# Optimization experiments

Measured on AMD Instinct MI355X. Metric: run time of the kernel, lower is better.

Reference implementation:

```python
import jax, jax.numpy as jnp
import numpy as np

N_HEAD, D_K, D_V, EPS = 8, 64, 64, 1e-6


def setup_inputs() -> dict:
    key = jax.random.key(0)
    ks = jax.random.split(key, 7)
    b, n, t, d = 8, 4, 512, 512
    q = jax.random.normal(ks[0], (b, n, t, d), dtype=jnp.float32)
    k = jax.random.normal(ks[1], (b, n, t, d), dtype=jnp.float32)
    v = jax.random.normal(ks[2], (b, n, t, d), dtype=jnp.float32)
    s = 1.0 / np.sqrt(d)
    w_q = jax.random.normal(ks[3], (N_HEAD * D_K, d), dtype=jnp.float32) * s
    w_k = jax.random.normal(ks[4], (N_HEAD * D_K, d), dtype=jnp.float32) * s
    w_v = jax.random.normal(ks[5], (N_HEAD * D_V, d), dtype=jnp.float32) * s
    w_fc = jax.random.normal(ks[6], (d, N_HEAD * D_V), dtype=jnp.float32) * s
    ln_gamma = jnp.ones((d,), dtype=jnp.float32)
    ln_beta = jnp.zeros((d,), dtype=jnp.float32)
    return {"q": q, "k": k, "v": v, "w_q": w_q, "w_k": w_k, "w_v": w_v,
            "w_fc": w_fc, "ln_gamma": ln_gamma, "ln_beta": ln_beta}


def reference(q, k, v, w_q, w_k, w_v, w_fc, ln_gamma, ln_beta):
    b, n, t, d = q.shape
    B = b * n
    qf = q.reshape(B, t, d)
    kf = k.reshape(B, t, d)
    vf = v.reshape(B, t, d)
    residual = qf
    # projections -> [B, H, T, dk/dv]
    Q = jnp.einsum('btd,ed->bte', qf, w_q).reshape(B, t, N_HEAD, D_K).transpose(0, 2, 1, 3)
    K = jnp.einsum('btd,ed->bte', kf, w_k).reshape(B, t, N_HEAD, D_K).transpose(0, 2, 1, 3)
    V = jnp.einsum('btd,ed->bte', vf, w_v).reshape(B, t, N_HEAD, D_V).transpose(0, 2, 1, 3)
    # scaled dot-product attention (scale by sqrt(d_k) of q's last dim)
    scale = 1.0 / jnp.sqrt(jnp.asarray(D_K, dtype=Q.dtype))
    attn = jax.nn.softmax(jnp.einsum('bhqd,bhkd->bhqk', Q * scale, K), axis=-1)
    O = jnp.einsum('bhqk,bhkd->bhqd', attn, V)  # [B, H, T, dv]
    # merge heads, then the original's extra transpose+view (layout scramble)
    x = O.transpose(0, 2, 1, 3).reshape(B, t, N_HEAD * D_V)
    x = jnp.transpose(x, (0, 2, 1)).reshape(B, t, N_HEAD * D_V)
    x = jnp.einsum('bte,de->btd', x, w_fc)
    x = x + residual
    # LayerNorm(eps=1e-6)
    mu = jnp.mean(x, axis=-1, keepdims=True)
    var = jnp.var(x, axis=-1, keepdims=True)
    x = (x - mu) * jax.lax.rsqrt(var + EPS) * ln_gamma + ln_beta
    return x.reshape(b, n, t, d)
```

## Files before the change

kernel.cpp:

```cpp
#include <hip/hip_runtime.h>
#include <hip/hip_bf16.h>
#include <stdint.h>

typedef __attribute__((ext_vector_type(8))) short bf16x8;
typedef __attribute__((ext_vector_type(4))) float f32x4;
typedef unsigned int u32;

#define MFMA16(a,b,c) __builtin_amdgcn_mfma_f32_16x16x32_bf16((a),(b),(c),0,0,0)

__device__ __forceinline__ unsigned short f2bf(float f) {
    unsigned u = __float_as_uint(f);
    u = (u + 0x7FFFu + ((u >> 16) & 1u)) >> 16;
    return (unsigned short)u;
}
__device__ __forceinline__ float bf2f(unsigned short h) {
    return __uint_as_float(((unsigned)h) << 16);
}
__device__ __forceinline__ void gload16(const unsigned short* gp, unsigned short* lp) {
    __builtin_amdgcn_global_load_lds(
        (const __attribute__((address_space(1))) u32*)gp,
        (__attribute__((address_space(3))) u32*)lp, 16, 0, 0);
}
__device__ __forceinline__ int xcd_swz(int bid, int q8) {
    return (bid & 7) * q8 + (bid >> 3);
}


__global__ __launch_bounds__(256) void prep_w(
    const float* __restrict__ wq, const float* __restrict__ wk, const float* __restrict__ wv,
    const float* __restrict__ wfc, unsigned short* __restrict__ Wcat)
{
    const int c = blockIdx.x * 256 + threadIdx.x;
    const int w = c >> 15;
    const long off = (long)(c & 32767) * 8;
    const float* src = (w == 0) ? wq : (w == 1) ? wk : (w == 2) ? wv : wfc;
    unsigned short* dst = Wcat + (long)w * 262144;
    const float4 a = *(const float4*)(src + off);
    const float4 b = *(const float4*)(src + off + 4);
    uint4 pk;
    pk.x = (u32)f2bf(a.x) | ((u32)f2bf(a.y) << 16);
    pk.y = (u32)f2bf(a.z) | ((u32)f2bf(a.w) << 16);
    pk.z = (u32)f2bf(b.x) | ((u32)f2bf(b.y) << 16);
    pk.w = (u32)f2bf(b.z) | ((u32)f2bf(b.w) << 16);
    *(uint4*)(dst + off) = pk;
}

__global__ __launch_bounds__(256) void proj_kernel(
    const float* __restrict__ qf, const float* __restrict__ kf, const float* __restrict__ vf,
    const unsigned short* __restrict__ Wcat,
    unsigned short* __restrict__ Qb, unsigned short* __restrict__ Kb,
    unsigned short* __restrict__ Vt)
{
    __shared__ __align__(16) unsigned short As[2][128 * 64];
    __shared__ __align__(16) unsigned short Bs[2][128 * 64];

    const int work = xcd_swz(blockIdx.x, 192);
    const int x = work & 3, y = (work >> 2) & 127, z = work >> 9;
    const float* Af = (z == 0) ? qf : (z == 1) ? kf : vf;
    const unsigned short* Bm = Wcat + (size_t)z * 262144;
    unsigned short* out = (z == 0) ? Qb : (z == 1) ? Kb : Vt;
    const int mode = (z == 2) ? 1 : 0;
    const float scale = (z == 0) ? 0.125f : 1.0f;
    const int m0 = y * 128, n0 = x * 128;

    const int tid = threadIdx.x, wid = tid >> 6, lane = tid & 63;
    const int wm = wid >> 1, wn = wid & 1;
    const int g = lane >> 4, cc = lane & 15;

    f32x4 acc[4][4];
    #pragma unroll
    for (int a = 0; a < 4; a++)
        #pragma unroll
        for (int b = 0; b < 4; b++)
            acc[a][b] = (f32x4){0.f, 0.f, 0.f, 0.f};

    int sslot[4], srow[4], scd[4];
    #pragma unroll
    for (int j = 0; j < 4; j++) {
        const int s = j * 256 + wid * 64 + lane;
        sslot[j] = s; srow[j] = s >> 3; scd[j] = (s & 7) ^ ((s >> 3) & 7);
    }

    float4 ra[8];
    auto LOADA = [&](int k0) {
        #pragma unroll
        for (int j = 0; j < 4; j++) {
            const float* src = Af + (size_t)(m0 + srow[j]) * 512 + k0 + scd[j] * 8;
            ra[2 * j]     = *(const float4*)src;
            ra[2 * j + 1] = *(const float4*)(src + 4);
        }
    };
    auto WRITEA = [&](unsigned short* Asb) {
        #pragma unroll
        for (int j = 0; j < 4; j++) {
            uint4 pk;
            pk.x = (u32)f2bf(ra[2 * j].x)     | ((u32)f2bf(ra[2 * j].y) << 16);
            pk.y = (u32)f2bf(ra[2 * j].z)     | ((u32)f2bf(ra[2 * j].w) << 16);
            pk.z = (u32)f2bf(ra[2 * j + 1].x) | ((u32)f2bf(ra[2 * j + 1].y) << 16);
            pk.w = (u32)f2bf(ra[2 * j + 1].z) | ((u32)f2bf(ra[2 * j + 1].w) << 16);
            *(uint4*)(Asb + (size_t)sslot[j] * 8) = pk;
        }
    };
    auto STAGEB = [&](unsigned short* Bsb, int k0) {
        #pragma unroll
        for (int j = 0; j < 4; j++) {
            const int sb = j * 256 + wid * 64;
            gload16(Bm + (size_t)(n0 + srow[j]) * 512 + k0 + scd[j] * 8,
                    Bsb + (size_t)sb * 8);
        }
    };

    LOADA(0); STAGEB(Bs[0], 0); WRITEA(As[0]);
    __syncthreads();

    #pragma unroll
    for (int t = 0; t < 8; t++) {
        unsigned short* Ac = As[t & 1];
        unsigned short* Bc = Bs[t & 1];
        if (t < 7) {
            LOADA((t + 1) * 64);
            STAGEB(Bs[(t + 1) & 1], (t + 1) * 64);
        }

        #pragma unroll
        for (int kc = 0; kc < 2; kc++) {
            bf16x8 af[4], bfr[4];
            #pragma unroll
            for (int mf = 0; mf < 4; mf++) {
                const int r = wm * 64 + mf * 16 + cc;
                af[mf] = *(const bf16x8*)(Ac + r * 64 + (((kc * 4 + g) ^ (r & 7)) * 8));
            }
            #pragma unroll
            for (int nf = 0; nf < 4; nf++) {
                const int r = wn * 64 + nf * 16 + cc;
                bfr[nf] = *(const bf16x8*)(Bc + r * 64 + (((kc * 4 + g) ^ (r & 7)) * 8));
            }
            __builtin_amdgcn_s_setprio(1);
            #pragma unroll
            for (int mf = 0; mf < 4; mf++)
                #pragma unroll
                for (int nf = 0; nf < 4; nf++)
                    acc[mf][nf] = MFMA16(af[mf], bfr[nf], acc[mf][nf]);
            __builtin_amdgcn_s_setprio(0);
        }
        if (t < 7) WRITEA(As[(t + 1) & 1]);
        __syncthreads();
    }

    #pragma unroll
    for (int mf = 0; mf < 4; mf++) {
        const int rg = m0 + wm * 64 + mf * 16 + g * 4;
        const int t0 = rg & 511, bI = rg >> 9;
        #pragma unroll
        for (int nf = 0; nf < 4; nf++) {
            const int col = n0 + wn * 64 + nf * 16 + cc;
            const int h = col >> 6, dd = col & 63;
            if (mode == 0) {
                const size_t base = ((size_t)((bI * 8 + h) * 512 + t0)) * 64 + dd;
                #pragma unroll
                for (int i = 0; i < 4; i++)
                    out[base + (size_t)i * 64] = f2bf(acc[mf][nf][i] * scale);
            } else {
                const size_t base = ((size_t)((bI * 8 + h) * 64 + dd)) * 512 + t0;
                uint2 pk;
                pk.x = (u32)f2bf(acc[mf][nf][0]) | ((u32)f2bf(acc[mf][nf][1]) << 16);
                pk.y = (u32)f2bf(acc[mf][nf][2]) | ((u32)f2bf(acc[mf][nf][3]) << 16);
                *(uint2*)(out + base) = pk;
            }
        }
    }
}

__global__ __launch_bounds__(256) void fc_kernel(
    const unsigned short* __restrict__ Os, const unsigned short* __restrict__ Wfc,
    unsigned short* __restrict__ Y)
{
    __shared__ __align__(16) unsigned short As[2][128 * 64];
    __shared__ __align__(16) unsigned short Bs[2][128 * 64];
    const int work = xcd_swz(blockIdx.x, 64);
    const int n0 = (work & 3) * 128, m0 = (work >> 2) * 128;

    const int tid = threadIdx.x, wid = tid >> 6, lane = tid & 63;
    const int wm = wid >> 1, wn = wid & 1;
    const int g = lane >> 4, cc = lane & 15;

    f32x4 acc[4][4];
    #pragma unroll
    for (int a = 0; a < 4; a++)
        #pragma unroll
        for (int b = 0; b < 4; b++)
            acc[a][b] = (f32x4){0.f, 0.f, 0.f, 0.f};

    auto STAGE = [&](unsigned short* Asb, unsigned short* Bsb, int k0) {
        #pragma unroll
        for (int j = 0; j < 4; j++) {
            const int sb = j * 256 + wid * 64;
            const int s = sb + lane;
            const int r = s >> 3;
            const int cd = (s & 7) ^ (r & 7);
            gload16(Os  + (size_t)(m0 + r) * 512 + k0 + cd * 8, Asb + (size_t)sb * 8);
            gload16(Wfc + (size_t)(n0 + r) * 512 + k0 + cd * 8, Bsb + (size_t)sb * 8);
        }
    };

    STAGE(As[0], Bs[0], 0);
    __syncthreads();

    #pragma unroll
    for (int t = 0; t < 8; t++) {
        unsigned short* Ac = As[t & 1];
        unsigned short* Bc = Bs[t & 1];
        if (t < 7) STAGE(As[(t + 1) & 1], Bs[(t + 1) & 1], (t + 1) * 64);

        #pragma unroll
        for (int kc = 0; kc < 2; kc++) {
            bf16x8 af[4], bfr[4];
            #pragma unroll
            for (int mf = 0; mf < 4; mf++) {
                const int r = wm * 64 + mf * 16 + cc;
                af[mf] = *(const bf16x8*)(Ac + r * 64 + (((kc * 4 + g) ^ (r & 7)) * 8));
            }
            #pragma unroll
            for (int nf = 0; nf < 4; nf++) {
                const int r = wn * 64 + nf * 16 + cc;
                bfr[nf] = *(const bf16x8*)(Bc + r * 64 + (((kc * 4 + g) ^ (r & 7)) * 8));
            }
            __builtin_amdgcn_s_setprio(1);
            #pragma unroll
            for (int mf = 0; mf < 4; mf++)
                #pragma unroll
                for (int nf = 0; nf < 4; nf++)
                    acc[mf][nf] = MFMA16(af[mf], bfr[nf], acc[mf][nf]);
            __builtin_amdgcn_s_setprio(0);
        }
        __syncthreads();
    }

    #pragma unroll
    for (int mf = 0; mf < 4; mf++) {
        const int rg = m0 + wm * 64 + mf * 16 + g * 4;
        #pragma unroll
        for (int nf = 0; nf < 4; nf++) {
            const int col = n0 + wn * 64 + nf * 16 + cc;
            #pragma unroll
            for (int i = 0; i < 4; i++)
                Y[(size_t)(rg + i) * 512 + col] = f2bf(acc[mf][nf][i]);
        }
    }
}

__global__ __launch_bounds__(256) void attn_kernel(
    const unsigned short* __restrict__ Qb, const unsigned short* __restrict__ Kb,
    const unsigned short* __restrict__ Vt, unsigned short* __restrict__ Os)
{
    __shared__ __align__(16) unsigned short Ks[64 * 64];
    __shared__ __align__(16) unsigned short Vs[64 * 64];
    __shared__ __align__(16) unsigned short Ps[4 * 32 * 64];

    const int work = xcd_swz(blockIdx.x, 128);
    const int qt = work & 3, bh = work >> 2;
    const int tid = threadIdx.x;
    const int wid = tid >> 6, lane = tid & 63;
    const int g = lane >> 4, cc = lane & 15;

    const unsigned short* Qp = Qb + (size_t)bh * 512 * 64;
    const unsigned short* Kp = Kb + (size_t)bh * 512 * 64;
    const unsigned short* Vp = Vt + (size_t)bh * 64 * 512;

    const int q0 = qt * 128 + wid * 32;

    bf16x8 qf[2][2];
    #pragma unroll
    for (int mf = 0; mf < 2; mf++)
        #pragma unroll
        for (int kb = 0; kb < 2; kb++)
            qf[mf][kb] = *(const bf16x8*)(Qp + (size_t)(q0 + mf * 16 + cc) * 64 + kb * 32 + g * 8);

    f32x4 o[2][4];
    #pragma unroll
    for (int a = 0; a < 2; a++)
        #pragma unroll
        for (int b = 0; b < 4; b++)
            o[a][b] = (f32x4){0.f, 0.f, 0.f, 0.f};
    float lrun[2][4];
    #pragma unroll
    for (int a = 0; a < 2; a++)
        #pragma unroll
        for (int i = 0; i < 4; i++) lrun[a][i] = 0.f;

    const int sb = wid * 64;
    const int s1 = sb + lane, r1 = s1 >> 3, cd1 = (s1 & 7) ^ (r1 & 7);
    const int s2 = sb + 256 + lane, r2 = s2 >> 3, cd2 = (s2 & 7) ^ (r2 & 7);

    for (int kt = 0; kt < 8; kt++) {
        gload16(Kp + (size_t)(kt * 64 + r1) * 64 + cd1 * 8, Ks + (size_t)sb * 8);
        gload16(Kp + (size_t)(kt * 64 + r2) * 64 + cd2 * 8, Ks + (size_t)(sb + 256) * 8);
        gload16(Vp + (size_t)r1 * 512 + kt * 64 + cd1 * 8, Vs + (size_t)sb * 8);
        gload16(Vp + (size_t)r2 * 512 + kt * 64 + cd2 * 8, Vs + (size_t)(sb + 256) * 8);
        __syncthreads();

        f32x4 s[2][4];
        #pragma unroll
        for (int a = 0; a < 2; a++)
            #pragma unroll
            for (int b = 0; b < 4; b++)
                s[a][b] = (f32x4){0.f, 0.f, 0.f, 0.f};
        __builtin_amdgcn_s_setprio(1);
        #pragma unroll
        for (int nf = 0; nf < 4; nf++) {
            const int r = nf * 16 + cc;
            #pragma unroll
            for (int kb = 0; kb < 2; kb++) {
                bf16x8 kf = *(const bf16x8*)(Ks + r * 64 + (((kb * 4 + g) ^ (r & 7)) * 8));
                s[0][nf] = MFMA16(qf[0][kb], kf, s[0][nf]);
                s[1][nf] = MFMA16(qf[1][kb], kf, s[1][nf]);
            }
        }
        __builtin_amdgcn_s_setprio(0);

        unsigned short* Pw = Ps + wid * 32 * 64;
        #pragma unroll
        for (int mf = 0; mf < 2; mf++)
            #pragma unroll
            for (int i = 0; i < 4; i++) {
                float lacc = 0.f;
                #pragma unroll
                for (int nf = 0; nf < 4; nf++) {
                    float p = __expf(s[mf][nf][i]);
                    s[mf][nf][i] = p;
                    lacc += p;
                }
                lrun[mf][i] += lacc;
            }

        #pragma unroll
        for (int mf = 0; mf < 2; mf++)
            #pragma unroll
            for (int nf = 0; nf < 4; nf++) {
                const int c = nf * 16 + cc, csl = c >> 3, cin = c & 7;
                #pragma unroll
                for (int i = 0; i < 4; i++) {
                    const int row = mf * 16 + g * 4 + i;
                    Pw[row * 64 + ((csl ^ (row & 7)) * 8) + cin] = f2bf(s[mf][nf][i]);
                }
            }

        __builtin_amdgcn_s_setprio(1);
        #pragma unroll
        for (int kc = 0; kc < 2; kc++) {
            bf16x8 pa[2], vb[4];
            #pragma unroll
            for (int mf = 0; mf < 2; mf++) {
                const int r = mf * 16 + cc;
                pa[mf] = *(const bf16x8*)(Pw + r * 64 + (((kc * 4 + g) ^ (r & 7)) * 8));
            }
            #pragma unroll
            for (int vf = 0; vf < 4; vf++) {
                const int r = vf * 16 + cc;
                vb[vf] = *(const bf16x8*)(Vs + r * 64 + (((kc * 4 + g) ^ (r & 7)) * 8));
            }
            #pragma unroll
            for (int mf = 0; mf < 2; mf++)
                #pragma unroll
                for (int vf = 0; vf < 4; vf++)
                    o[mf][vf] = MFMA16(pa[mf], vb[vf], o[mf][vf]);
        }
        __builtin_amdgcn_s_setprio(0);
        __syncthreads();
    }

    const int b = bh >> 3, h = bh & 7;
    #pragma unroll
    for (int mf = 0; mf < 2; mf++) {
        int tq0 = q0 + mf * 16 + g * 4;
        float inv[4];
        #pragma unroll
        for (int i = 0; i < 4; i++) {
            float l = lrun[mf][i];
            #pragma unroll
            for (int d = 1; d < 16; d <<= 1) l += __shfl_xor(l, d);
            inv[i] = 1.0f / l;
        }
        #pragma unroll
        for (int vf = 0; vf < 4; vf++) {
            int dv = vf * 16 + cc;
            uint2 pk;
            pk.x = (u32)f2bf(o[mf][vf][0] * inv[0]) | ((u32)f2bf(o[mf][vf][1] * inv[1]) << 16);
            pk.y = (u32)f2bf(o[mf][vf][2] * inv[2]) | ((u32)f2bf(o[mf][vf][3] * inv[3]) << 16);
            size_t base = ((size_t)b * 512 + h * 64 + dv) * 512 + tq0;
            *(uint2*)(Os + base) = pk;
        }
    }
}

__global__ __launch_bounds__(256) void ln_kernel(
    const unsigned short* __restrict__ y, const float* __restrict__ resid,
    const float* __restrict__ gamma, const float* __restrict__ beta,
    float* __restrict__ out)
{
    const int wid = threadIdx.x >> 6, lane = threadIdx.x & 63;
    const int row = blockIdx.x * 4 + wid;
    const unsigned short* yr = y + (size_t)row * 512;
    const float* rr = resid + (size_t)row * 512;

    const bf16x8 yv = *(const bf16x8*)(yr + lane * 8);
    const float4 r0 = *(const float4*)(rr + lane * 8);
    const float4 r1 = *(const float4*)(rr + lane * 8 + 4);
    float x[8];
    x[0] = bf2f((unsigned short)yv[0]) + r0.x;
    x[1] = bf2f((unsigned short)yv[1]) + r0.y;
    x[2] = bf2f((unsigned short)yv[2]) + r0.z;
    x[3] = bf2f((unsigned short)yv[3]) + r0.w;
    x[4] = bf2f((unsigned short)yv[4]) + r1.x;
    x[5] = bf2f((unsigned short)yv[5]) + r1.y;
    x[6] = bf2f((unsigned short)yv[6]) + r1.z;
    x[7] = bf2f((unsigned short)yv[7]) + r1.w;

    float s = 0.f, sq = 0.f;
    #pragma unroll
    for (int j = 0; j < 8; j++) { s += x[j]; sq += x[j] * x[j]; }
    #pragma unroll
    for (int d = 1; d < 64; d <<= 1) {
        s += __shfl_xor(s, d);
        sq += __shfl_xor(sq, d);
    }
    const float mu = s * (1.0f / 512.0f);
    const float var = sq * (1.0f / 512.0f) - mu * mu;
    const float rs = rsqrtf(var + 1e-6f);

    #pragma unroll
    for (int j = 0; j < 2; j++) {
        const int colb = lane * 8 + j * 4;
        const float4 gg = *(const float4*)(gamma + colb);
        const float4 bb = *(const float4*)(beta + colb);
        float4 ov;
        ov.x = (x[j * 4 + 0] - mu) * rs * gg.x + bb.x;
        ov.y = (x[j * 4 + 1] - mu) * rs * gg.y + bb.y;
        ov.z = (x[j * 4 + 2] - mu) * rs * gg.z + bb.z;
        ov.w = (x[j * 4 + 3] - mu) * rs * gg.w + bb.w;
        *(float4*)(out + (size_t)row * 512 + colb) = ov;
    }
}

extern "C" void kernel_launch(void* const* d_in, const int* in_sizes, int n_in,
                              void* d_out, int out_size, void* d_ws, size_t ws_size,
                              hipStream_t stream) {
    const float* q     = (const float*)d_in[0];
    const float* k     = (const float*)d_in[1];
    const float* v     = (const float*)d_in[2];
    const float* wq    = (const float*)d_in[3];
    const float* wk    = (const float*)d_in[4];
    const float* wv    = (const float*)d_in[5];
    const float* wfc   = (const float*)d_in[6];
    const float* gamma = (const float*)d_in[7];
    const float* beta  = (const float*)d_in[8];
    float* out = (float*)d_out;

    char* ws = (char*)d_ws;
    const size_t SEG = 16777216;
    unsigned short* Qb   = (unsigned short*)(ws);
    unsigned short* Kb   = (unsigned short*)(ws + SEG);
    unsigned short* Vt   = (unsigned short*)(ws + 2 * SEG);
    unsigned short* Os   = (unsigned short*)(ws + 3 * SEG);
    unsigned short* Y    = (unsigned short*)(ws + 4 * SEG);
    unsigned short* Wcat = (unsigned short*)(ws + 5 * SEG);

    prep_w<<<512, 256, 0, stream>>>(wq, wk, wv, wfc, Wcat);
    proj_kernel<<<1536, 256, 0, stream>>>(q, k, v, Wcat, Qb, Kb, Vt);
    attn_kernel<<<1024, 256, 0, stream>>>(Qb, Kb, Vt, Os);
    fc_kernel<<<512, 256, 0, stream>>>(Os, Wcat + 786432, Y);
    ln_kernel<<<4096, 256, 0, stream>>>(Y, q, gamma, beta, out);
}
```

Measured before the change: 125.8 us.

## Prefetch A tiles two steps ahead with register double-buffering and explicit waitcnt

The projection GEMM kernel now keeps two register buffers for the fp32 A tile and issues A loads two k-steps ahead, while B is still staged one step ahead via direct-to-LDS loads. Partial vmcnt waits and sched_barriers replace __syncthreads so the in-flight loads for the far tile can stay outstanding across the barrier. The aim is to hide global load latency of the fp32 activations behind MFMA work. The cost is extra VGPR pressure from a second 8xfloat4 buffer, plus reliance on hand-counted vmcnt values being correct.

```diff
diff --git a/kernel.cpp b/kernel.cpp
--- a/kernel.cpp
+++ b/kernel.cpp
@@ -81,8 +81,8 @@
         sslot[j] = s; srow[j] = s >> 3; scd[j] = (s & 7) ^ ((s >> 3) & 7);
     }
 
-    float4 ra[8];
-    auto LOADA = [&](int k0) {
+    float4 raA[8], raB[8];
+    auto LOADA = [&](float4* ra, int k0) {
         #pragma unroll
         for (int j = 0; j < 4; j++) {
             const float* src = Af + (size_t)(m0 + srow[j]) * 512 + k0 + scd[j] * 8;
@@ -90,7 +90,7 @@
             ra[2 * j + 1] = *(const float4*)(src + 4);
         }
     };
-    auto WRITEA = [&](unsigned short* Asb) {
+    auto WRITEA = [&](const float4* ra, unsigned short* Asb) {
         #pragma unroll
         for (int j = 0; j < 4; j++) {
             uint4 pk;
@@ -110,17 +110,27 @@
         }
     };
 
-    LOADA(0); STAGEB(Bs[0], 0); WRITEA(As[0]);
-    __syncthreads();
+    LOADA(raA, 0);
+    STAGEB(Bs[0], 0);
+    LOADA(raB, 64);
+    WRITEA(raA, As[0]);
+    asm volatile("s_waitcnt vmcnt(8) lgkmcnt(0)" ::: "memory");
+    __builtin_amdgcn_sched_barrier(0);
+    __builtin_amdgcn_s_barrier();
+    __builtin_amdgcn_sched_barrier(0);
 
     #pragma unroll
     for (int t = 0; t < 8; t++) {
-        unsigned short* Ac = As[t & 1];
-        unsigned short* Bc = Bs[t & 1];
-        if (t < 7) {
-            LOADA((t + 1) * 64);
-            STAGEB(Bs[(t + 1) & 1], (t + 1) * 64);
-        }
+        const int cur = t & 1;
+        float4* rnext = (t & 1) ? raA : raB;
+        float4* rfar  = (t & 1) ? raB : raA;
+        if (t < 6) {
+            STAGEB(Bs[cur ^ 1], (t + 1) * 64);
+            LOADA(rfar, (t + 2) * 64);
+        } else if (t == 6) {
+            STAGEB(Bs[1], 7 * 64);
+        }
+        __builtin_amdgcn_sched_barrier(0);
 
         #pragma unroll
         for (int kc = 0; kc < 2; kc++) {
@@ -128,12 +138,12 @@
             #pragma unroll
             for (int mf = 0; mf < 4; mf++) {
                 const int r = wm * 64 + mf * 16 + cc;
-                af[mf] = *(const bf16x8*)(Ac + r * 64 + (((kc * 4 + g) ^ (r & 7)) * 8));
+                af[mf] = *(const bf16x8*)(As[cur] + r * 64 + (((kc * 4 + g) ^ (r & 7)) * 8));
             }
             #pragma unroll
             for (int nf = 0; nf < 4; nf++) {
                 const int r = wn * 64 + nf * 16 + cc;
-                bfr[nf] = *(const bf16x8*)(Bc + r * 64 + (((kc * 4 + g) ^ (r & 7)) * 8));
+                bfr[nf] = *(const bf16x8*)(Bs[cur] + r * 64 + (((kc * 4 + g) ^ (r & 7)) * 8));
             }
             __builtin_amdgcn_s_setprio(1);
             #pragma unroll
@@ -143,8 +153,18 @@
                     acc[mf][nf] = MFMA16(af[mf], bfr[nf], acc[mf][nf]);
             __builtin_amdgcn_s_setprio(0);
         }
-        if (t < 7) WRITEA(As[(t + 1) & 1]);
-        __syncthreads();
+
+        if (t < 7) {
+            __builtin_amdgcn_sched_barrier(0);
+            WRITEA(rnext, As[cur ^ 1]);
+            if (t < 6)
+                asm volatile("s_waitcnt vmcnt(8) lgkmcnt(0)" ::: "memory");
+            else
+                asm volatile("s_waitcnt vmcnt(0) lgkmcnt(0)" ::: "memory");
+            __builtin_amdgcn_sched_barrier(0);
+            __builtin_amdgcn_s_barrier();
+            __builtin_amdgcn_sched_barrier(0);
+        }
     }
 
     #pragma unroll
```

Result: no change. 123.9 us (-1.6%).

## Stage fp32 activations directly to LDS via async loads in projection GEMM

Applied to the files above, without the earlier changes.

The projection kernel now stages fp32 activation tiles straight into shared memory with global_load_lds instead of loading them to registers, converting and writing bf16. Conversion to bf16 moves to fragment-read time. The K step halves to 32 with 16 iterations, swizzles are redone for the new tile shapes, and launch bounds request 3 blocks per CU. This is meant to cut register pressure and let the A loads overlap asynchronously, at the cost of more LDS traffic, repeated conversion work per fragment read, and twice as many barriers.

```diff
diff --git a/kernel.cpp b/kernel.cpp
--- a/kernel.cpp
+++ b/kernel.cpp
@@ -17,6 +17,11 @@
     return __uint_as_float(((unsigned)h) << 16);
 }
 __device__ __forceinline__ void gload16(const unsigned short* gp, unsigned short* lp) {
+    __builtin_amdgcn_global_load_lds(
+        (const __attribute__((address_space(1))) u32*)gp,
+        (__attribute__((address_space(3))) u32*)lp, 16, 0, 0);
+}
+__device__ __forceinline__ void gload16f(const float* gp, float* lp) {
     __builtin_amdgcn_global_load_lds(
         (const __attribute__((address_space(1))) u32*)gp,
         (__attribute__((address_space(3))) u32*)lp, 16, 0, 0);
@@ -45,14 +50,14 @@
     *(uint4*)(dst + off) = pk;
 }
 
-__global__ __launch_bounds__(256) void proj_kernel(
+__global__ __launch_bounds__(256, 3) void proj_kernel(
     const float* __restrict__ qf, const float* __restrict__ kf, const float* __restrict__ vf,
     const unsigned short* __restrict__ Wcat,
     unsigned short* __restrict__ Qb, unsigned short* __restrict__ Kb,
     unsigned short* __restrict__ Vt)
 {
-    __shared__ __align__(16) unsigned short As[2][128 * 64];
-    __shared__ __align__(16) unsigned short Bs[2][128 * 64];
+    __shared__ __align__(16) float          Afp[2][128 * 32];
+    __shared__ __align__(16) unsigned short Bsm[2][128 * 32];
 
     const int work = xcd_swz(blockIdx.x, 192);
     const int x = work & 3, y = (work >> 2) & 127, z = work >> 9;
@@ -74,76 +79,60 @@
         for (int b = 0; b < 4; b++)
             acc[a][b] = (f32x4){0.f, 0.f, 0.f, 0.f};
 
-    int sslot[4], srow[4], scd[4];
-    #pragma unroll
-    for (int j = 0; j < 4; j++) {
-        const int s = j * 256 + wid * 64 + lane;
-        sslot[j] = s; srow[j] = s >> 3; scd[j] = (s & 7) ^ ((s >> 3) & 7);
-    }
-
-    float4 ra[8];
-    auto LOADA = [&](int k0) {
-        #pragma unroll
-        for (int j = 0; j < 4; j++) {
-            const float* src = Af + (size_t)(m0 + srow[j]) * 512 + k0 + scd[j] * 8;
-            ra[2 * j]     = *(const float4*)src;
-            ra[2 * j + 1] = *(const float4*)(src + 4);
-        }
-    };
-    auto WRITEA = [&](unsigned short* Asb) {
-        #pragma unroll
-        for (int j = 0; j < 4; j++) {
-            uint4 pk;
-            pk.x = (u32)f2bf(ra[2 * j].x)     | ((u32)f2bf(ra[2 * j].y) << 16);
-            pk.y = (u32)f2bf(ra[2 * j].z)     | ((u32)f2bf(ra[2 * j].w) << 16);
-            pk.z = (u32)f2bf(ra[2 * j + 1].x) | ((u32)f2bf(ra[2 * j + 1].y) << 16);
-            pk.w = (u32)f2bf(ra[2 * j + 1].z) | ((u32)f2bf(ra[2 * j + 1].w) << 16);
-            *(uint4*)(Asb + (size_t)sslot[j] * 8) = pk;
-        }
-    };
-    auto STAGEB = [&](unsigned short* Bsb, int k0) {
+    auto STAGE = [&](float* Ab, unsigned short* Bb, int k0) {
         #pragma unroll
         for (int j = 0; j < 4; j++) {
             const int sb = j * 256 + wid * 64;
-            gload16(Bm + (size_t)(n0 + srow[j]) * 512 + k0 + scd[j] * 8,
-                    Bsb + (size_t)sb * 8);
+            const int s = sb + lane;
+            const int r = s >> 3, cs = s & 7;
+            const int cd = cs ^ (r & 7);
+            gload16f(Af + (size_t)(m0 + r) * 512 + k0 + cd * 4, Ab + (size_t)sb * 4);
+        }
+        #pragma unroll
+        for (int j = 0; j < 2; j++) {
+            const int sb = j * 256 + wid * 64;
+            const int s = sb + lane;
+            const int r = s >> 2, cs = s & 3;
+            const int cd = cs ^ ((r >> 1) & 3);
+            gload16(Bm + (size_t)(n0 + r) * 512 + k0 + cd * 8, Bb + (size_t)sb * 8);
         }
     };
 
-    LOADA(0); STAGEB(Bs[0], 0); WRITEA(As[0]);
+    STAGE(Afp[0], Bsm[0], 0);
     __syncthreads();
 
-    #pragma unroll
-    for (int t = 0; t < 8; t++) {
-        unsigned short* Ac = As[t & 1];
-        unsigned short* Bc = Bs[t & 1];
-        if (t < 7) {
-            LOADA((t + 1) * 64);
-            STAGEB(Bs[(t + 1) & 1], (t + 1) * 64);
-        }
-
-        #pragma unroll
-        for (int kc = 0; kc < 2; kc++) {
-            bf16x8 af[4], bfr[4];
-            #pragma unroll
-            for (int mf = 0; mf < 4; mf++) {
-                const int r = wm * 64 + mf * 16 + cc;
-                af[mf] = *(const bf16x8*)(Ac + r * 64 + (((kc * 4 + g) ^ (r & 7)) * 8));
-            }
-            #pragma unroll
-            for (int nf = 0; nf < 4; nf++) {
-                const int r = wn * 64 + nf * 16 + cc;
-                bfr[nf] = *(const bf16x8*)(Bc + r * 64 + (((kc * 4 + g) ^ (r & 7)) * 8));
-            }
-            __builtin_amdgcn_s_setprio(1);
-            #pragma unroll
-            for (int mf = 0; mf < 4; mf++)
-                #pragma unroll
-                for (int nf = 0; nf < 4; nf++)
-                    acc[mf][nf] = MFMA16(af[mf], bfr[nf], acc[mf][nf]);
-            __builtin_amdgcn_s_setprio(0);
-        }
-        if (t < 7) WRITEA(As[(t + 1) & 1]);
+    #pragma unroll 2
+    for (int t = 0; t < 16; t++) {
+        const int cur = t & 1;
+        if (t < 15) STAGE(Afp[cur ^ 1], Bsm[cur ^ 1], (t + 1) * 32);
+
+        bf16x8 af[4], bfr[4];
+        #pragma unroll
+        for (int mf = 0; mf < 4; mf++) {
+            const int r = wm * 64 + mf * 16 + cc;
+            const int s0 = (2 * g) ^ (r & 7), s1 = (2 * g + 1) ^ (r & 7);
+            const float4 lo = *(const float4*)(&Afp[cur][r * 32 + s0 * 4]);
+            const float4 hi = *(const float4*)(&Afp[cur][r * 32 + s1 * 4]);
+            bf16x8 v;
+            v[0] = (short)f2bf(lo.x); v[1] = (short)f2bf(lo.y);
+            v[2] = (short)f2bf(lo.z); v[3] = (short)f2bf(lo.w);
+            v[4] = (short)f2bf(hi.x); v[5] = (short)f2bf(hi.y);
+            v[6] = (short)f2bf(hi.z); v[7] = (short)f2bf(hi.w);
+            af[mf] = v;
+        }
+        #pragma unroll
+        for (int nf = 0; nf < 4; nf++) {
+            const int r = wn * 64 + nf * 16 + cc;
+            const int sl = g ^ ((r >> 1) & 3);
+            bfr[nf] = *(const bf16x8*)(&Bsm[cur][r * 32 + sl * 8]);
+        }
+        __builtin_amdgcn_s_setprio(1);
+        #pragma unroll
+        for (int mf = 0; mf < 4; mf++)
+            #pragma unroll
+            for (int nf = 0; nf < 4; nf++)
+                acc[mf][nf] = MFMA16(af[mf], bfr[nf], acc[mf][nf]);
+        __builtin_amdgcn_s_setprio(0);
         __syncthreads();
     }
 
```

Measured after the change: 123.2 us. -2.1%, faster.
